# Optimization experiments

Hardware: AMD Instinct MI355X
Metric: run time of the kernel (lower is better)

## Reference

```python
import jax, jax.numpy as jnp
import numpy as np

B, L, FD = 16, 196, 2048      # batch, fmap locations (14x14), resnet101 feat dim
N, WD, HD, DD = 1000, 300, 512, 5  # n_class, word_dim, hid_dim, d_dim
E, TMAX, NIMG = 50000, 5, 1000     # n_edges, gru steps, imagenet classes


def setup_inputs():
    key = jax.random.key(0)
    ks = jax.random.split(key, 32)
    p = lambda k, s: (jax.random.normal(k, s, jnp.float32) * 0.02)
    z = lambda n: jnp.zeros((n,), jnp.float32)
    return {
        'feats': jax.random.normal(ks[0], (B, L, FD), jnp.float32),
        'embed': jax.random.normal(ks[1], (N, WD), jnp.float32),
        'edges': jax.random.randint(ks[2], (2, E), 0, N, jnp.int32),
        # attention key/query nets
        'W_key': p(ks[3], (FD, HD)), 'b_key': z(HD),
        'W_query': p(ks[4], (WD, HD)), 'b_query': z(HD),
        # F_in: feat_dim -> 512 -> d_dim (relu)
        'Wf1': p(ks[5], (FD, 512)), 'bf1': z(512),
        'Wf2': p(ks[6], (512, DD)), 'bf2': z(DD),
        # F_rel: 2*word_dim -> 256 -> 1 (relu)
        'Wr1': p(ks[7], (2 * WD, 256)), 'br1': z(256),
        'Wr2': p(ks[8], (256, 1)), 'br2': z(1),
        # F_out: d_dim -> 512 -> 1 (relu)
        'Wo1': p(ks[9], (DD, 512)), 'bo1': z(512),
        'Wo2': p(ks[10], (512, 1)), 'bo2': z(1),
        # GRUCell (torch layout: [3*d, d] stacked r,z,n)
        'W_ih': p(ks[11], (3 * DD, DD)), 'b_ih': z(3 * DD),
        'W_hh': p(ks[12], (3 * DD, DD)), 'b_hh': z(3 * DD),
        # imagenet classifier on pooled features
        'W_clf': p(ks[13], (FD, NIMG)), 'b_clf': z(NIMG),
    }


def _gru_cell(x, h, W_ih, W_hh, b_ih, b_hh):
    gi = x @ W_ih.T + b_ih            # [M, 3d]
    gh = h @ W_hh.T + b_hh
    i_r, i_z, i_n = jnp.split(gi, 3, axis=-1)
    h_r, h_z, h_n = jnp.split(gh, 3, axis=-1)
    r = jax.nn.sigmoid(i_r + h_r)
    zg = jax.nn.sigmoid(i_z + h_z)
    n = jnp.tanh(i_n + r * h_n)
    return (1.0 - zg) * n + zg * h


def reference(feats, embed, edges, W_key, b_key, W_query, b_query,
              Wf1, bf1, Wf2, bf2, Wr1, br1, Wr2, br2, Wo1, bo1, Wo2, bo2,
              W_ih, b_ih, W_hh, b_hh, W_clf, b_clf):
    # imagenet scores from globally pooled backbone features
    pooled = jnp.mean(feats, axis=1)                      # [B, FD]
    imgnet_scores = jax.nn.softmax(pooled @ W_clf + b_clf, axis=1)

    # label-conditional spatial attention
    keys = feats @ W_key + b_key                          # [B, L, HD]
    queries = embed @ W_query + b_query                   # [N, HD]
    scores = jnp.einsum('blh,nh->bnl', keys, queries)     # [B, N, L]
    attn = jax.nn.softmax(scores, axis=2)
    graph_input = jnp.einsum('bnl,blf->bnf', attn, feats) # [B, N, FD]
    graph_input = graph_input.reshape(-1, FD)             # [B*N, FD]

    # F_in MLP -> initial hidden state
    h0 = jax.nn.relu(graph_input @ Wf1 + bf1) @ Wf2 + bf2  # [B*N, DD]

    # edge weights from word-embedding pairs, scattered into dense [N, N]
    et = jnp.concatenate([embed[edges[0]], embed[edges[1]]], axis=1)  # [E, 2*WD]
    vals = jnp.tanh((jax.nn.relu(et @ Wr1 + br1) @ Wr2 + br2).reshape(-1))
    prop_mat = jnp.zeros((N, N), jnp.float32).at[edges[0], edges[1]].add(vals)

    # t_max message-passing + GRU steps (sequential recurrence)
    def step(hidden, _):
        msg = jnp.tanh(jnp.einsum('nm,bmd->bnd', prop_mat,
                                  hidden.reshape(B, N, DD))).reshape(-1, DD)
        return _gru_cell(msg, hidden, W_ih, W_hh, b_ih, b_hh), None
    hidden, _ = jax.lax.scan(step, h0, None, length=TMAX)

    logits = (jax.nn.relu(hidden @ Wo1 + bo1) @ Wo2 + bo2).reshape(B, N)
    return logits, attn, imgnet_scores
```

## Files before the change

### kernel.cpp

```cpp
#include <hip/hip_runtime.h>
#include <hip/hip_bf16.h>
#include <math.h>

#define B_   16
#define L_   196
#define FD_  2048
#define N_   1000
#define WD_  300
#define HD_  512
#define DD_  5
#define E_   50000
#define TMAX_ 5
#define NIMG_ 1000
#define WDP_ 320
#define LP_  224
#define EKP_ 640

typedef __attribute__((ext_vector_type(8))) short bf16x8;
typedef __attribute__((ext_vector_type(4))) float f32x4;

#define SMEM_MEGA1    49152
#define SMEM_MM_SPLIT 49152
#define SMEM_MM_NS    24576
#define SMEM_PREP     4352

#define SBAR()    asm volatile("s_barrier" ::: "memory")
#define WVM(N)    asm volatile("s_waitcnt vmcnt(" #N ")" ::: "memory")

__device__ __forceinline__ short bf_hi(float x) {
    unsigned u = __float_as_uint(x);
    unsigned r = u + 0x7fffu + ((u >> 16) & 1u);
    return (short)(r >> 16);
}
__device__ __forceinline__ float bf2f_(short s) {
    return __uint_as_float(((unsigned)(unsigned short)s) << 16);
}

__device__ __forceinline__ void gl16(const short* g, char* l) {
    __builtin_amdgcn_global_load_lds(
        (const __attribute__((address_space(1))) void*)g,
        (__attribute__((address_space(3))) void*)l, 16, 0, 0);
}

#define OUT_SPLIT 1
#define OUT_SC    2
#define OUT_F1T   3
#define OUT_H0    4

template<int OUTMODE, bool SPLIT>
__device__ __forceinline__ void mm_core(
    char* sm, int bx, int by, int zb,
    const short* __restrict__ Ah, const short* __restrict__ Al,
    const short* __restrict__ Bh, const short* __restrict__ Bl,
    const float* __restrict__ bias, void* __restrict__ C0, void* __restrict__ C1,
    void* __restrict__ C2, const float* __restrict__ W2,
    int M, int N, int K, int kbeg, int kend)
{
    const int PBUF = SPLIT ? 24576 : 12288;
    char* AsH = sm;
    char* AsL = sm + 8192;
    char* BsH = sm + (SPLIT ? 16384 : 8192);
    char* BsL = sm + 20480;
    int t = threadIdx.x;
    int lane = t & 63, w = t >> 6;
    int q = lane >> 4, r = lane & 15;
    int row0 = by * 128, col0 = bx * 64;

    int srow = t >> 2, cd = t & 3;
    int cg = cd ^ ((srow >> 1) & 3);
    int gA0 = row0 + srow;       if (gA0 >= M) gA0 = M - 1;
    int gA1 = row0 + 64 + srow;  if (gA1 >= M) gA1 = M - 1;
    int gB  = col0 + srow;       if (gB  >= N) gB  = N - 1;
    const short* pA0 = Ah + (long)gA0 * K + cg * 8 + kbeg;
    const short* pA1 = Ah + (long)gA1 * K + cg * 8 + kbeg;
    const short* pB  = Bh + (long)gB  * K + cg * 8 + kbeg;
    const short* pA0l = Ah; const short* pA1l = Ah; const short* pBl = Bh;
    if (SPLIT) {
        pA0l = Al + (long)gA0 * K + cg * 8 + kbeg;
        pA1l = Al + (long)gA1 * K + cg * 8 + kbeg;
        pBl  = Bl + (long)gB  * K + cg * 8 + kbeg;
    }
    char* dA0 = AsH + t * 16;
    char* dA1 = AsH + 4096 + t * 16;
    char* dB  = BsH + t * 16;
    char* dA0l = AsL + t * 16;
    char* dA1l = AsL + 4096 + t * 16;
    char* dBl  = BsL + t * 16;

    int x = (q ^ ((r >> 1) & 3)) * 16;
    int aoff0 = (w * 32 + r) * 64 + x;
    int aoff1 = aoff0 + 1024;
    int boff[4];
    #pragma unroll
    for (int ct = 0; ct < 4; ct++) boff[ct] = (ct * 16 + r) * 64 + x;

    f32x4 zero4 = {0.f, 0.f, 0.f, 0.f};
    f32x4 acc[2][4];
    #pragma unroll
    for (int i = 0; i < 2; i++)
        #pragma unroll
        for (int j = 0; j < 4; j++) acc[i][j] = zero4;

    auto stage = [&](int ks) {
        int off = (ks & 1) * PBUF;
        int ko = ks * 32;
        gl16(pA0 + ko, dA0 + off);
        gl16(pA1 + ko, dA1 + off);
        gl16(pB  + ko, dB  + off);
        if (SPLIT) {
            gl16(pA0l + ko, dA0l + off);
            gl16(pA1l + ko, dA1l + off);
            gl16(pBl  + ko, dBl  + off);
        }
    };

    int nk = (kend - kbeg) >> 5;
    stage(0);
    for (int ks = 0; ks < nk; ks++) {
        if (ks + 1 < nk) {
            stage(ks + 1);
            if (SPLIT) { WVM(6); } else { WVM(3); }
        } else {
            WVM(0);
        }
        SBAR();

        int cur = (ks & 1) * PBUF;
        bf16x8 ah0 = *(const bf16x8*)(AsH + cur + aoff0);
        bf16x8 ah1 = *(const bf16x8*)(AsH + cur + aoff1);
        bf16x8 al0, al1;
        if (SPLIT) {
            al0 = *(const bf16x8*)(AsL + cur + aoff0);
            al1 = *(const bf16x8*)(AsL + cur + aoff1);
        }
        #pragma unroll
        for (int ct = 0; ct < 4; ct++) {
            bf16x8 bh = *(const bf16x8*)(BsH + cur + boff[ct]);
            acc[0][ct] = __builtin_amdgcn_mfma_f32_16x16x32_bf16(ah0, bh, acc[0][ct], 0, 0, 0);
            acc[1][ct] = __builtin_amdgcn_mfma_f32_16x16x32_bf16(ah1, bh, acc[1][ct], 0, 0, 0);
            if (SPLIT) {
                acc[0][ct] = __builtin_amdgcn_mfma_f32_16x16x32_bf16(al0, bh, acc[0][ct], 0, 0, 0);
                acc[1][ct] = __builtin_amdgcn_mfma_f32_16x16x32_bf16(al1, bh, acc[1][ct], 0, 0, 0);
                bf16x8 bl = *(const bf16x8*)(BsL + cur + boff[ct]);
                acc[0][ct] = __builtin_amdgcn_mfma_f32_16x16x32_bf16(ah0, bl, acc[0][ct], 0, 0, 0);
                acc[1][ct] = __builtin_amdgcn_mfma_f32_16x16x32_bf16(ah1, bl, acc[1][ct], 0, 0, 0);
            }
        }
        if (ks + 1 < nk) SBAR();
    }

    if (OUTMODE == OUT_H0) {
        float s[2][4][DD_];
        #pragma unroll
        for (int i = 0; i < 2; i++)
            #pragma unroll
            for (int reg = 0; reg < 4; reg++)
                #pragma unroll
                for (int d = 0; d < DD_; d++) s[i][reg][d] = 0.f;
        #pragma unroll
        for (int i = 0; i < 2; i++) {
            #pragma unroll
            for (int ct = 0; ct < 4; ct++) {
                int n = col0 + ct * 16 + r;
                float w2v[DD_];
                #pragma unroll
                for (int d = 0; d < DD_; d++) w2v[d] = W2[n * DD_ + d];
                float b1 = bias[n];
                #pragma unroll
                for (int reg = 0; reg < 4; reg++) {
                    int m = row0 + w * 32 + i * 16 + q * 4 + reg;
                    if (m >= M) continue;
                    float val = fmaxf(acc[i][ct][reg] + b1, 0.f);
                    #pragma unroll
                    for (int d = 0; d < DD_; d++) s[i][reg][d] = fmaf(val, w2v[d], s[i][reg][d]);
                }
            }
        }
        #pragma unroll
        for (int i = 0; i < 2; i++)
            #pragma unroll
            for (int reg = 0; reg < 4; reg++)
                #pragma unroll
                for (int d = 0; d < DD_; d++) {
                    float v = s[i][reg][d];
                    v += __shfl_xor(v, 1);
                    v += __shfl_xor(v, 2);
                    v += __shfl_xor(v, 4);
                    v += __shfl_xor(v, 8);
                    if (r == 0) {
                        int m = row0 + w * 32 + i * 16 + q * 4 + reg;
                        if (m < M)
                            atomicAdd(&((float*)C0)[(long)m * (B_ * DD_) + zb * DD_ + d], v);
                    }
                }
        return;
    }

    #pragma unroll
    for (int i = 0; i < 2; i++) {
        #pragma unroll
        for (int ct = 0; ct < 4; ct++) {
            #pragma unroll
            for (int reg = 0; reg < 4; reg++) {
                int m = row0 + w * 32 + i * 16 + q * 4 + reg;
                int n = col0 + ct * 16 + r;
                if (m >= M || n >= N) continue;
                float v = acc[i][ct][reg];
                if (OUTMODE == OUT_SC) {
                    ((float*)C0)[(long)m * N + n] = v;
                } else if (OUTMODE == OUT_F1T) {
                    int b = m / 196, l = m - b * 196;
                    ((short*)C2)[((long)b * 512 + n) * LP_ + l] = bf_hi(v);
                } else {
                    float v2 = v + bias[n];
                    long idx = (long)m * N + n;
                    short hi = bf_hi(v2);
                    ((short*)C0)[idx] = hi;
                    ((short*)C1)[idx] = bf_hi(v2 - bf2f_(hi));
                }
            }
        }
    }
}

__device__ __forceinline__ void edge_core(
    char* sm, int be,
    const short* __restrict__ embedH, const int* __restrict__ edges,
    const short* __restrict__ Wr1T, const float* __restrict__ br1,
    const float* __restrict__ Wr2, const float* __restrict__ br2,
    float* __restrict__ prop)
{
    const int EPBUF = 20480;
    char* As = sm;
    char* Bs = sm + 4096;
    int* src = (int*)(sm + 40960);
    int* dst = (int*)(sm + 41216);
    float (*part)[5] = (float(*)[5])(sm + 41472);
    int t = threadIdx.x;
    int e0 = be * 64;
    if (t < 64) {
        int e = e0 + t;
        src[t] = (e < E_) ? edges[e] : 0;
        dst[t] = (e < E_) ? edges[E_ + e] : 0;
    }
    __syncthreads();
    int lane = t & 63, w = t >> 6, q = lane >> 4, r = lane & 15;
    f32x4 zero4 = {0.f, 0.f, 0.f, 0.f};
    f32x4 acc[4][4];
    #pragma unroll
    for (int i = 0; i < 4; i++)
        #pragma unroll
        for (int j = 0; j < 4; j++) acc[i][j] = zero4;

    int srow = t >> 2, cd = t & 3;
    int cg = cd ^ ((srow >> 1) & 3);
    const short* baseS = embedH + (long)src[srow] * WDP_ + cg * 8;
    const short* baseD = embedH + (long)dst[srow] * WDP_ + cg * 8;
    const short* pB = Wr1T + (long)srow * EKP_ + cg * 8;
    char* dA = As + t * 16;
    char* dB = Bs + t * 16;

    int x = (q ^ ((r >> 1) & 3)) * 16;
    int aoff[4], boff[4];
    #pragma unroll
    for (int i = 0; i < 4; i++) {
        aoff[i] = (i * 16 + r) * 64 + x;
        boff[i] = (w * 64 + i * 16 + r) * 64 + x;
    }

    auto estage = [&](int ks) {
        int off = (ks & 1) * EPBUF;
        const short* pa = (ks < 10) ? baseS + ks * 32 : baseD + (ks - 10) * 32;
        gl16(pa, dA + off);
        #pragma unroll
        for (int i = 0; i < 4; i++)
            gl16(pB + (long)i * 64 * EKP_ + ks * 32, dB + i * 4096 + off);
    };

    estage(0);
    for (int ks = 0; ks < 20; ks++) {
        if (ks + 1 < 20) {
            estage(ks + 1);
            WVM(5);
        } else {
            WVM(0);
        }
        SBAR();

        int cur = (ks & 1) * EPBUF;
        bf16x8 af[4], bfr[4];
        #pragma unroll
        for (int rt = 0; rt < 4; rt++) af[rt] = *(const bf16x8*)(As + cur + aoff[rt]);
        #pragma unroll
        for (int ct = 0; ct < 4; ct++) bfr[ct] = *(const bf16x8*)(Bs + cur + boff[ct]);
        #pragma unroll
        for (int rt = 0; rt < 4; rt++)
            #pragma unroll
            for (int ct = 0; ct < 4; ct++)
                acc[rt][ct] = __builtin_amdgcn_mfma_f32_16x16x32_bf16(af[rt], bfr[ct], acc[rt][ct], 0, 0, 0);
        if (ks + 1 < 20) SBAR();
    }
    float b1v[4], w2v[4];
    #pragma unroll
    for (int ct = 0; ct < 4; ct++) {
        int u = w * 64 + ct * 16 + r;
        b1v[ct] = br1[u];
        w2v[ct] = Wr2[u];
    }
    #pragma unroll
    for (int rt = 0; rt < 4; rt++) {
        #pragma unroll
        for (int reg = 0; reg < 4; reg++) {
            float s = 0.f;
            #pragma unroll
            for (int ct = 0; ct < 4; ct++)
                s = fmaf(fmaxf(acc[rt][ct][reg] + b1v[ct], 0.f), w2v[ct], s);
            s += __shfl_xor(s, 1);
            s += __shfl_xor(s, 2);
            s += __shfl_xor(s, 4);
            s += __shfl_xor(s, 8);
            if (r == 0) part[rt * 16 + q * 4 + reg][w] = s;
        }
    }
    __syncthreads();
    if (t < 64 && e0 + t < E_) {
        float s = part[t][0] + part[t][1] + part[t][2] + part[t][3];
        atomicAdd(&prop[(long)src[t] * N_ + dst[t]], tanhf(s + br2[0]));
    }
}

__device__ __forceinline__ void transconv_core(
    char* sm, int bx, int by,
    const float* __restrict__ in, short* __restrict__ outH, short* __restrict__ outL,
    int Kd, int N, int Ks)
{
    float (*tile)[33] = (float(*)[33])sm;
    int k0 = bx * 32, n0 = by * 32;
    int t = threadIdx.x;
    int tr = t >> 5, tc = t & 31;
    #pragma unroll
    for (int i = 0; i < 4; i++) {
        int k = k0 + tr + i * 8, n = n0 + tc;
        tile[tr + i * 8][tc] = (k < Kd && n < N) ? in[(long)k * N + n] : 0.f;
    }
    __syncthreads();
    #pragma unroll
    for (int i = 0; i < 4; i++) {
        int n = n0 + tr + i * 8, k = k0 + tc;
        if (n < N && k < Ks) {
            float x = tile[tc][tr + i * 8];
            short hi = bf_hi(x);
            outH[(long)n * Ks + k] = hi;
            if (outL) outL[(long)n * Ks + k] = bf_hi(x - bf2f_(hi));
        }
    }
}

__global__ __launch_bounds__(256) void prep(
    float* __restrict__ prop, float* __restrict__ Ht0, const float* __restrict__ bf2,
    const float* __restrict__ feats, float* __restrict__ pooled,
    short* __restrict__ featsH, short* __restrict__ featsL,
    const float* __restrict__ embed, short* __restrict__ embH, short* __restrict__ embL,
    const float* __restrict__ W_key, const float* __restrict__ Wf1,
    short* __restrict__ WkfH, short* __restrict__ WkfL,
    const float* __restrict__ W_query, short* __restrict__ WqTh, short* __restrict__ WqTl,
    const float* __restrict__ Wr1, short* __restrict__ Wr1T, short* __restrict__ F1T)
{
    __shared__ __align__(16) char sm[SMEM_PREP];
    int b = blockIdx.x, t = threadIdx.x;
    if (b < 977) {
        int i = (b * 256 + t) * 4;
        if (i < N_ * N_) { float4 z = {0.f, 0.f, 0.f, 0.f}; *(float4*)(prop + i) = z; }
    } else if (b < 1290) {
        int i = (b - 977) * 256 + t;
        if (i < N_ * B_ * DD_) Ht0[i] = bf2[i % DD_];
    } else if (b < 1418) {
        int idx = (b - 1290) * 256 + t;
        int bb = idx / FD_, f = idx % FD_;
        const float* p = feats + (long)bb * L_ * FD_ + f;
        float acc = 0.f;
        for (int l = 0; l < L_; l++) acc += p[(long)l * FD_];
        pooled[idx] = acc * (1.0f / L_);
    } else if (b < 4554) {
        long i = ((long)(b - 1418) * 256 + t) * 8;
        float4 v0 = *(const float4*)(feats + i);
        float4 v1 = *(const float4*)(feats + i + 4);
        float xs[8] = {v0.x, v0.y, v0.z, v0.w, v1.x, v1.y, v1.z, v1.w};
        short h[8], l8[8];
        #pragma unroll
        for (int j = 0; j < 8; j++) {
            h[j] = bf_hi(xs[j]);
            l8[j] = bf_hi(xs[j] - bf2f_(h[j]));
        }
        *(int4*)(featsH + i) = *(int4*)h;
        *(int4*)(featsL + i) = *(int4*)l8;
    } else if (b < 4867) {
        int i = ((b - 4554) * 256 + t) * 4;
        if (i < N_ * WDP_) {
            int n = i / WDP_, c = i - n * WDP_;
            short h[4], l4[4];
            if (c < WD_) {
                float4 v = *(const float4*)(embed + (long)n * WD_ + c);
                float xs[4] = {v.x, v.y, v.z, v.w};
                #pragma unroll
                for (int j = 0; j < 4; j++) {
                    h[j] = bf_hi(xs[j]);
                    l4[j] = bf_hi(xs[j] - bf2f_(h[j]));
                }
            } else {
                #pragma unroll
                for (int j = 0; j < 4; j++) { h[j] = 0; l4[j] = 0; }
            }
            *(int2*)(embH + (long)n * WDP_ + c) = *(int2*)h;
            *(int2*)(embL + (long)n * WDP_ + c) = *(int2*)l4;
        }
    } else if (b < 5891) {
        int bb = b - 4867;
        transconv_core(sm, bb % 64, bb / 64, W_key, WkfH, WkfL, FD_, HD_, FD_);
    } else if (b < 6915) {
        int bb = b - 5891;
        transconv_core(sm, bb % 64, bb / 64, Wf1, WkfH + (size_t)512 * FD_, nullptr, FD_, HD_, FD_);
    } else if (b < 7075) {
        int bb = b - 6915;
        transconv_core(sm, bb % 10, bb / 10, W_query, WqTh, WqTl, WD_, HD_, WDP_);
    } else if (b < 7235) {
        int bb = b - 7075;
        int bx = bb % 20, by = bb / 20;
        float (*tile)[33] = (float(*)[33])sm;
        int k0 = bx * 32, n0 = by * 32;
        int tr = t >> 5, tc = t & 31;
        #pragma unroll
        for (int i = 0; i < 4; i++) {
            int kout = k0 + tr + i * 8, n = n0 + tc;
            int kin = (kout < 320) ? kout : kout - 20;
            bool valid = (kout < 320) ? (kout < 300) : (kout < 620);
            tile[tr + i * 8][tc] = valid ? Wr1[(long)kin * 256 + n] : 0.f;
        }
        __syncthreads();
        #pragma unroll
        for (int i = 0; i < 4; i++) {
            int n = n0 + tr + i * 8, k = k0 + tc;
            Wr1T[(long)n * EKP_ + k] = bf_hi(tile[tc][tr + i * 8]);
        }
    } else {
        long i = ((long)(b - 7235) * 256 + t) * 8;
        int4 z = {0, 0, 0, 0};
        *(int4*)(F1T + i) = z;
    }
}

__global__ __launch_bounds__(256) void mega1(
    const short* __restrict__ featsH, const short* __restrict__ featsL,
    const short* __restrict__ WkfH, const short* __restrict__ WkfL,
    const float* __restrict__ b_key, short* __restrict__ keysH, short* __restrict__ keysL,
    short* __restrict__ F1T,
    const short* __restrict__ embH, const short* __restrict__ embL,
    const short* __restrict__ WqTh, const short* __restrict__ WqTl,
    const float* __restrict__ b_query, short* __restrict__ qH, short* __restrict__ qL,
    const int* __restrict__ edges, const short* __restrict__ Wr1T,
    const float* __restrict__ br1, const float* __restrict__ Wr2,
    const float* __restrict__ br2, float* __restrict__ prop,
    const float* __restrict__ pooled, const float* __restrict__ W_clf,
    const float* __restrict__ b_clf, float* __restrict__ Pimg)
{
    __shared__ __align__(16) char sm[SMEM_MEGA1];
    int b = blockIdx.x;
    if (b < 200) {
        int l = (b & 7) * 25 + (b >> 3);
        mm_core<OUT_SPLIT, true>(sm, l & 7, l >> 3, 0,
            featsH, featsL, WkfH, WkfL, b_key,
            keysH, keysL, nullptr, nullptr, B_ * L_, 512, FD_, 0, FD_);
    } else if (b < 400) {
        int bb = b - 200;
        int l = (bb & 7) * 25 + (bb >> 3);
        mm_core<OUT_F1T, false>(sm, l & 7, l >> 3, 0,
            featsH, nullptr, WkfH + (size_t)512 * FD_, nullptr, nullptr,
            nullptr, nullptr, F1T, nullptr, B_ * L_, 512, FD_, 0, FD_);
    } else if (b < 464) {
        int bb = b - 400;
        int l = (bb & 7) * 8 + (bb >> 3);
        mm_core<OUT_SPLIT, true>(sm, l & 7, l >> 3, 0,
            embH, embL, WqTh, WqTl, b_query,
            qH, qL, nullptr, nullptr, N_, HD_, WDP_, 0, WDP_);
    } else if (b < 1246) {
        edge_core(sm, b - 464, embH, edges, Wr1T, br1, Wr2, br2, prop);
    } else {
        int bb = b - 1246;
        int ks = bb / 63, ix = bb % 63;
        int i = ix * 256 + threadIdx.x;
        if (i < B_ * NIMG_) {
            int bi = i / NIMG_, n = i % NIMG_;
            const float* p = pooled + (long)bi * FD_ + ks * 256;
            const float* w = W_clf + (long)(ks * 256) * NIMG_ + n;
            float acc = (ks == 0) ? b_clf[n] : 0.f;
            #pragma unroll 4
            for (int k = 0; k < 256; k++) acc = fmaf(p[k], w[(long)k * NIMG_], acc);
            Pimg[(long)ks * (B_ * NIMG_) + i] = acc;
        }
    }
}

__global__ __launch_bounds__(256) void mega2(
    const short* __restrict__ qH, const short* __restrict__ qL,
    const short* __restrict__ keysH, const short* __restrict__ keysL,
    float* __restrict__ Pattn,
    const float* __restrict__ Pimg, float* __restrict__ out_img)
{
    __shared__ __align__(16) char sm[SMEM_MM_SPLIT];
    int b = blockIdx.x;
    if (b < 1024) {
        int l = (b & 7) * 128 + (b >> 3);
        int zb = l >> 6, by = (l >> 3) & 7, kc = (l >> 2) & 1, bx = l & 3;
        const short* Bh = keysH + (long)zb * L_ * HD_;
        const short* Bl = keysL + (long)zb * L_ * HD_;
        float* C0 = Pattn + (long)kc * ((long)B_ * N_ * L_) + (long)zb * N_ * L_;
        mm_core<OUT_SC, true>(sm, bx, by, 0, qH, qL, Bh, Bl, nullptr,
                              C0, nullptr, nullptr, nullptr,
                              N_, L_, HD_, kc * 256, kc * 256 + 256);
    } else {
        int t = threadIdx.x;
        int wave = (b - 1024) * 4 + (t >> 6), lane = t & 63;
        if (wave >= B_) return;
        const int PER = (NIMG_ + 63) / 64;
        float v[PER];
        float m = -1e30f;
        int cnt = 0;
        for (int k = lane; k < NIMG_; k += 64) {
            float s = 0.f;
            #pragma unroll
            for (int ks = 0; ks < 8; ks++) s += Pimg[(long)ks * (B_ * NIMG_) + wave * NIMG_ + k];
            v[cnt] = s; m = fmaxf(m, s); cnt++;
        }
        #pragma unroll
        for (int off = 32; off; off >>= 1) m = fmaxf(m, __shfl_xor(m, off));
        float s = 0.f;
        for (int i = 0; i < cnt; i++) { v[i] = expf(v[i] - m); s += v[i]; }
        #pragma unroll
        for (int off = 32; off; off >>= 1) s += __shfl_xor(s, off);
        float inv = 1.f / s;
        cnt = 0;
        for (int k = lane; k < NIMG_; k += 64) out_img[(long)wave * NIMG_ + k] = v[cnt++] * inv;
    }
}

__global__ void softmax_attn(const float* __restrict__ P0, const float* __restrict__ P1,
                             float* __restrict__ X, short* __restrict__ Xb, int rows)
{
    int gid = blockIdx.x * blockDim.x + threadIdx.x;
    int wave = gid >> 6, lane = gid & 63;
    if (wave >= rows) return;
    const int PER = (L_ + 63) / 64;
    float v[PER];
    float m = -1e30f;
    int cnt = 0;
    for (int k = lane; k < L_; k += 64) {
        long idx = (long)wave * L_ + k;
        v[cnt] = P0[idx] + P1[idx];
        m = fmaxf(m, v[cnt]); cnt++;
    }
    #pragma unroll
    for (int off = 32; off; off >>= 1) m = fmaxf(m, __shfl_xor(m, off));
    float s = 0.f;
    for (int i = 0; i < cnt; i++) { v[i] = expf(v[i] - m); s += v[i]; }
    #pragma unroll
    for (int off = 32; off; off >>= 1) s += __shfl_xor(s, off);
    float inv = 1.f / s;
    cnt = 0;
    for (int k = lane; k < L_; k += 64) {
        float val = v[cnt++] * inv;
        X[(long)wave * L_ + k] = val;
        Xb[(long)wave * LP_ + k] = bf_hi(val);
    }
    if (lane < LP_ - L_) Xb[(long)wave * LP_ + L_ + lane] = 0;
}

__global__ __launch_bounds__(256) void h0gemm(
    const short* __restrict__ attnH, const short* __restrict__ F1T,
    const float* __restrict__ bf1, const float* __restrict__ Wf2,
    float* __restrict__ Ht0)
{
    __shared__ __align__(16) char sm[SMEM_MM_NS];
    int b = blockIdx.x;
    int l = (b & 7) * 128 + (b >> 3);
    int zb = l >> 6, by = (l >> 3) & 7, bx = l & 7;
    const short* Ap = attnH + (long)zb * N_ * LP_;
    const short* Bp = F1T + (long)zb * HD_ * LP_;
    mm_core<OUT_H0, false>(sm, bx, by, zb, Ap, nullptr, Bp, nullptr,
                           bf1, Ht0, nullptr, nullptr, Wf2,
                           N_, HD_, LP_, 0, LP_);
}

__global__ __launch_bounds__(320) void step_kernel(
    const float* __restrict__ prop, const float* __restrict__ Hin,
    float* __restrict__ Hout,
    const float* __restrict__ W_ih, const float* __restrict__ b_ih,
    const float* __restrict__ W_hh, const float* __restrict__ b_hh)
{
    __shared__ float msg[4][80];
    int t = threadIdx.x;
    int nl = t / 80, c = t - nl * 80;
    int n = blockIdx.x * 4 + nl;
    const float* pr = prop + (long)n * N_;
    const float* hc = Hin + c;
    float acc = 0.f;
    #pragma unroll 4
    for (int m4 = 0; m4 < N_; m4 += 4) {
        float4 pv = *(const float4*)(pr + m4);
        acc = fmaf(pv.x, hc[(long)(m4 + 0) * 80], acc);
        acc = fmaf(pv.y, hc[(long)(m4 + 1) * 80], acc);
        acc = fmaf(pv.z, hc[(long)(m4 + 2) * 80], acc);
        acc = fmaf(pv.w, hc[(long)(m4 + 3) * 80], acc);
    }
    msg[nl][c] = tanhf(acc);
    __syncthreads();
    if (t < 64) {
        int nl2 = t >> 4, b = t & 15;
        int n2 = blockIdx.x * 4 + nl2;
        float xv[DD_], h[DD_];
        #pragma unroll
        for (int j = 0; j < DD_; j++) {
            xv[j] = msg[nl2][b * DD_ + j];
            h[j] = Hin[(long)n2 * 80 + b * DD_ + j];
        }
        float gi[3 * DD_], gh[3 * DD_];
        #pragma unroll
        for (int g = 0; g < 3 * DD_; g++) {
            float a = b_ih[g], cc = b_hh[g];
            #pragma unroll
            for (int k = 0; k < DD_; k++) {
                a = fmaf(xv[k], W_ih[g * DD_ + k], a);
                cc = fmaf(h[k], W_hh[g * DD_ + k], cc);
            }
            gi[g] = a; gh[g] = cc;
        }
        #pragma unroll
        for (int j = 0; j < DD_; j++) {
            float rr = 1.f / (1.f + expf(-(gi[j] + gh[j])));
            float zz = 1.f / (1.f + expf(-(gi[DD_ + j] + gh[DD_ + j])));
            float nn2 = tanhf(gi[2 * DD_ + j] + rr * gh[2 * DD_ + j]);
            Hout[(long)n2 * 80 + b * DD_ + j] = (1.f - zz) * nn2 + zz * h[j];
        }
    }
}

__global__ void out_kernel(const float* __restrict__ ht, const float* __restrict__ Wo1,
                           const float* __restrict__ bo1, const float* __restrict__ Wo2,
                           const float* __restrict__ bo2, float* __restrict__ logits, int rows)
{
    int gid = blockIdx.x * blockDim.x + threadIdx.x;
    int wave = gid >> 6, lane = gid & 63;
    if (wave >= rows) return;
    int b = wave / N_, n = wave % N_;
    float x[DD_];
    #pragma unroll
    for (int i = 0; i < DD_; i++) x[i] = ht[(long)n * (B_ * DD_) + b * DD_ + i];
    float acc = 0.f;
    for (int j = lane; j < HD_; j += 64) {
        float h = bo1[j];
        #pragma unroll
        for (int d = 0; d < DD_; d++) h = fmaf(x[d], Wo1[d * HD_ + j], h);
        h = fmaxf(h, 0.f);
        acc = fmaf(h, Wo2[j], acc);
    }
    #pragma unroll
    for (int off = 32; off; off >>= 1) acc += __shfl_down(acc, off);
    if (lane == 0) logits[wave] = acc + bo2[0];
}

extern "C" void kernel_launch(void* const* d_in, const int* in_sizes, int n_in,
                              void* d_out, int out_size, void* d_ws, size_t ws_size,
                              hipStream_t stream)
{
    const float* feats   = (const float*)d_in[0];
    const float* embed   = (const float*)d_in[1];
    const int*   edges   = (const int*)  d_in[2];
    const float* W_key   = (const float*)d_in[3];
    const float* b_key   = (const float*)d_in[4];
    const float* W_query = (const float*)d_in[5];
    const float* b_query = (const float*)d_in[6];
    const float* Wf1     = (const float*)d_in[7];
    const float* bf1     = (const float*)d_in[8];
    const float* Wf2     = (const float*)d_in[9];
    const float* bf2     = (const float*)d_in[10];
    const float* Wr1     = (const float*)d_in[11];
    const float* br1     = (const float*)d_in[12];
    const float* Wr2     = (const float*)d_in[13];
    const float* br2     = (const float*)d_in[14];
    const float* Wo1     = (const float*)d_in[15];
    const float* bo1     = (const float*)d_in[16];
    const float* Wo2     = (const float*)d_in[17];
    const float* bo2     = (const float*)d_in[18];
    const float* W_ih    = (const float*)d_in[19];
    const float* b_ih    = (const float*)d_in[20];
    const float* W_hh    = (const float*)d_in[21];
    const float* b_hh    = (const float*)d_in[22];
    const float* W_clf   = (const float*)d_in[23];
    const float* b_clf   = (const float*)d_in[24];

    float* out_logits = (float*)d_out;
    float* out_attn   = out_logits + B_ * N_;
    float* out_img    = out_attn + (long)B_ * N_ * L_;

    char* p = (char*)d_ws;
    auto alloc = [&](size_t bytes) { void* r = (void*)p; p += (bytes + 255) & ~(size_t)255; return r; };
    float* pooled  = (float*)alloc((size_t)B_ * FD_ * 4);
    short* featsH  = (short*)alloc((size_t)B_ * L_ * FD_ * 2);
    short* featsL  = (short*)alloc((size_t)B_ * L_ * FD_ * 2);
    short* WkfH    = (short*)alloc((size_t)1024 * FD_ * 2);
    short* WkfL    = (short*)alloc((size_t)512 * FD_ * 2);
    short* WqTh    = (short*)alloc((size_t)HD_ * WDP_ * 2);
    short* WqTl    = (short*)alloc((size_t)HD_ * WDP_ * 2);
    short* Wr1T    = (short*)alloc((size_t)256 * EKP_ * 2);
    short* embH    = (short*)alloc((size_t)N_ * WDP_ * 2);
    short* embL    = (short*)alloc((size_t)N_ * WDP_ * 2);
    short* keysH   = (short*)alloc((size_t)B_ * L_ * HD_ * 2);
    short* keysL   = (short*)alloc((size_t)B_ * L_ * HD_ * 2);
    short* qH      = (short*)alloc((size_t)N_ * HD_ * 2);
    short* qL      = (short*)alloc((size_t)N_ * HD_ * 2);
    short* attnH   = (short*)alloc((size_t)B_ * N_ * LP_ * 2);
    short* F1T     = (short*)alloc((size_t)B_ * HD_ * LP_ * 2);
    float* prop    = (float*)alloc((size_t)N_ * N_ * 4);
    float* Ht0     = (float*)alloc((size_t)N_ * B_ * DD_ * 4);
    float* Ht1     = (float*)alloc((size_t)N_ * B_ * DD_ * 4);
    float* Pimg    = (float*)alloc((size_t)8 * B_ * NIMG_ * 4);
    float* Pattn   = (float*)alloc((size_t)2 * B_ * N_ * L_ * 4);

    prep<<<8131, 256, 0, stream>>>(prop, Ht0, bf2, feats, pooled, featsH, featsL,
                                   embed, embH, embL, W_key, Wf1, WkfH, WkfL,
                                   W_query, WqTh, WqTl, Wr1, Wr1T, F1T);

    mega1<<<1750, 256, 0, stream>>>(featsH, featsL, WkfH, WkfL, b_key, keysH, keysL, F1T,
                                    embH, embL, WqTh, WqTl, b_query, qH, qL,
                                    edges, Wr1T, br1, Wr2, br2, prop,
                                    pooled, W_clf, b_clf, Pimg);

    mega2<<<1028, 256, 0, stream>>>(qH, qL, keysH, keysL, Pattn, Pimg, out_img);

    softmax_attn<<<(B_ * N_ * 64 + 255) / 256, 256, 0, stream>>>(
        Pattn, Pattn + (long)B_ * N_ * L_, out_attn, attnH, B_ * N_);

    h0gemm<<<1024, 256, 0, stream>>>(attnH, F1T, bf1, Wf2, Ht0);

    {
        float* hin = Ht0;
        float* hout = Ht1;
        for (int step = 0; step < TMAX_; step++) {
            step_kernel<<<N_ / 4, 320, 0, stream>>>(prop, hin, hout,
                                                    W_ih, b_ih, W_hh, b_hh);
            float* tmp = hin; hin = hout; hout = tmp;
        }
        out_kernel<<<(B_ * N_ * 64 + 255) / 256, 256, 0, stream>>>(hin, Wo1, bo1, Wo2, bo2,
                                                                   out_logits, B_ * N_);
    }
}
```

Baseline: 524.0 us.

## Drop split-K in score GEMM, split step kernel reduction, shrink F1T zeroing

The attention score GEMM no longer splits K into two halves, so it writes one partial buffer instead of two and the softmax reads a single input. The recurrent step kernel now uses 640 threads, splitting the 1000-long message reduction into two halves with four independent accumulators each, combined through shared memory before tanh. The F1T zero-fill in prep now clears only the padded tail columns (196..223) of each row instead of the whole buffer, which reduces the grid size. The trade-off is fewer GEMM blocks and less parallelism for the score stage, in exchange for less memory traffic and a shorter dependency chain in the latency-bound recurrence.

```diff
diff --git a/kernel.cpp b/kernel.cpp
--- a/kernel.cpp
+++ b/kernel.cpp
@@ -443,9 +443,10 @@
             Wr1T[(long)n * EKP_ + k] = bf_hi(tile[tc][tr + i * 8]);
         }
     } else {
-        long i = ((long)(b - 7235) * 256 + t) * 8;
-        int4 z = {0, 0, 0, 0};
-        *(int4*)(F1T + i) = z;
+        int idx = (b - 7235) * 256 + t;
+        int row = idx / 7, j = idx - row * 7;
+        int2 z2; z2.x = 0; z2.y = 0;
+        *(int2*)(F1T + (long)row * LP_ + 196 + j * 4) = z2;
     }
 }
 
@@ -508,18 +509,18 @@
 {
     __shared__ __align__(16) char sm[SMEM_MM_SPLIT];
     int b = blockIdx.x;
-    if (b < 1024) {
-        int l = (b & 7) * 128 + (b >> 3);
-        int zb = l >> 6, by = (l >> 3) & 7, kc = (l >> 2) & 1, bx = l & 3;
+    if (b < 512) {
+        int l = (b & 7) * 64 + (b >> 3);
+        int zb = l >> 5, by = (l >> 2) & 7, bx = l & 3;
         const short* Bh = keysH + (long)zb * L_ * HD_;
         const short* Bl = keysL + (long)zb * L_ * HD_;
-        float* C0 = Pattn + (long)kc * ((long)B_ * N_ * L_) + (long)zb * N_ * L_;
+        float* C0 = Pattn + (long)zb * N_ * L_;
         mm_core<OUT_SC, true>(sm, bx, by, 0, qH, qL, Bh, Bl, nullptr,
                               C0, nullptr, nullptr, nullptr,
-                              N_, L_, HD_, kc * 256, kc * 256 + 256);
+                              N_, L_, HD_, 0, HD_);
     } else {
         int t = threadIdx.x;
-        int wave = (b - 1024) * 4 + (t >> 6), lane = t & 63;
+        int wave = (b - 512) * 4 + (t >> 6), lane = t & 63;
         if (wave >= B_) return;
         const int PER = (NIMG_ + 63) / 64;
         float v[PER];
@@ -543,7 +544,7 @@
     }
 }
 
-__global__ void softmax_attn(const float* __restrict__ P0, const float* __restrict__ P1,
+__global__ void softmax_attn(const float* __restrict__ P0,
                              float* __restrict__ X, short* __restrict__ Xb, int rows)
 {
     int gid = blockIdx.x * blockDim.x + threadIdx.x;
@@ -554,8 +555,7 @@
     float m = -1e30f;
     int cnt = 0;
     for (int k = lane; k < L_; k += 64) {
-        long idx = (long)wave * L_ + k;
-        v[cnt] = P0[idx] + P1[idx];
+        v[cnt] = P0[(long)wave * L_ + k];
         m = fmaxf(m, v[cnt]); cnt++;
     }
     #pragma unroll
@@ -590,28 +590,34 @@
                            N_, HD_, LP_, 0, LP_);
 }
 
-__global__ __launch_bounds__(320) void step_kernel(
+__global__ __launch_bounds__(640) void step_kernel(
     const float* __restrict__ prop, const float* __restrict__ Hin,
     float* __restrict__ Hout,
     const float* __restrict__ W_ih, const float* __restrict__ b_ih,
     const float* __restrict__ W_hh, const float* __restrict__ b_hh)
 {
-    __shared__ float msg[4][80];
+    __shared__ float msg[2][4][80];
     int t = threadIdx.x;
-    int nl = t / 80, c = t - nl * 80;
+    int half = t / 320, tt = t - half * 320;
+    int nl = tt / 80, c = tt - nl * 80;
     int n = blockIdx.x * 4 + nl;
-    const float* pr = prop + (long)n * N_;
-    const float* hc = Hin + c;
-    float acc = 0.f;
+    const float* pr = prop + (long)n * N_ + half * 500;
+    const float* hc = Hin + c + (long)half * 500 * 80;
+    float a0 = 0.f, a1 = 0.f, a2 = 0.f, a3 = 0.f;
     #pragma unroll 4
-    for (int m4 = 0; m4 < N_; m4 += 4) {
+    for (int m4 = 0; m4 < 500; m4 += 4) {
         float4 pv = *(const float4*)(pr + m4);
-        acc = fmaf(pv.x, hc[(long)(m4 + 0) * 80], acc);
-        acc = fmaf(pv.y, hc[(long)(m4 + 1) * 80], acc);
-        acc = fmaf(pv.z, hc[(long)(m4 + 2) * 80], acc);
-        acc = fmaf(pv.w, hc[(long)(m4 + 3) * 80], acc);
-    }
-    msg[nl][c] = tanhf(acc);
+        a0 = fmaf(pv.x, hc[(long)(m4 + 0) * 80], a0);
+        a1 = fmaf(pv.y, hc[(long)(m4 + 1) * 80], a1);
+        a2 = fmaf(pv.z, hc[(long)(m4 + 2) * 80], a2);
+        a3 = fmaf(pv.w, hc[(long)(m4 + 3) * 80], a3);
+    }
+    msg[half][nl][c] = (a0 + a1) + (a2 + a3);
+    __syncthreads();
+    if (t < 320) {
+        int nl2 = t / 80, c2 = t - nl2 * 80;
+        msg[0][nl2][c2] = tanhf(msg[0][nl2][c2] + msg[1][nl2][c2]);
+    }
     __syncthreads();
     if (t < 64) {
         int nl2 = t >> 4, b = t & 15;
@@ -619,7 +625,7 @@
         float xv[DD_], h[DD_];
         #pragma unroll
         for (int j = 0; j < DD_; j++) {
-            xv[j] = msg[nl2][b * DD_ + j];
+            xv[j] = msg[0][nl2][b * DD_ + j];
             h[j] = Hin[(long)n2 * 80 + b * DD_ + j];
         }
         float gi[3 * DD_], gh[3 * DD_];
@@ -723,9 +729,9 @@
     float* Ht0     = (float*)alloc((size_t)N_ * B_ * DD_ * 4);
     float* Ht1     = (float*)alloc((size_t)N_ * B_ * DD_ * 4);
     float* Pimg    = (float*)alloc((size_t)8 * B_ * NIMG_ * 4);
-    float* Pattn   = (float*)alloc((size_t)2 * B_ * N_ * L_ * 4);
-
-    prep<<<8131, 256, 0, stream>>>(prop, Ht0, bf2, feats, pooled, featsH, featsL,
+    float* Pattn   = (float*)alloc((size_t)B_ * N_ * L_ * 4);
+
+    prep<<<7459, 256, 0, stream>>>(prop, Ht0, bf2, feats, pooled, featsH, featsL,
                                    embed, embH, embL, W_key, Wf1, WkfH, WkfL,
                                    W_query, WqTh, WqTl, Wr1, Wr1T, F1T);
 
@@ -734,10 +740,10 @@
                                     edges, Wr1T, br1, Wr2, br2, prop,
                                     pooled, W_clf, b_clf, Pimg);
 
-    mega2<<<1028, 256, 0, stream>>>(qH, qL, keysH, keysL, Pattn, Pimg, out_img);
+    mega2<<<516, 256, 0, stream>>>(qH, qL, keysH, keysL, Pattn, Pimg, out_img);
 
     softmax_attn<<<(B_ * N_ * 64 + 255) / 256, 256, 0, stream>>>(
-        Pattn, Pattn + (long)B_ * N_ * L_, out_attn, attnH, B_ * N_);
+        Pattn, out_attn, attnH, B_ * N_);
 
     h0gemm<<<1024, 256, 0, stream>>>(attnH, F1T, bf1, Wf2, Ht0);
 
@@ -745,7 +751,7 @@
         float* hin = Ht0;
         float* hout = Ht1;
         for (int step = 0; step < TMAX_; step++) {
-            step_kernel<<<N_ / 4, 320, 0, stream>>>(prop, hin, hout,
+            step_kernel<<<N_ / 4, 640, 0, stream>>>(prop, hin, hout,
                                                     W_ih, b_ih, W_hh, b_hh);
             float* tmp = hin; hin = hout; hout = tmp;
         }
```

New measurement: 439.4 us, median of 2. -16.1%, faster.
